# Optimization experiments

Measured on AMD Instinct MI355X. Metric: run time of the kernel, lower is better.

Reference implementation:

```python
import jax, jax.numpy as jnp
import numpy as np

B, L1, L2, DIN, H, DK, DV = 16, 1024, 1024, 1024, 16, 64, 64


def setup_inputs() -> dict:
    key = jax.random.key(0)
    ks = jax.random.split(key, 9)
    s = 1.0 / np.sqrt(DIN)
    return {
        "x": jax.random.normal(ks[0], (B, L1, DIN), dtype=jnp.float32),
        "y": jax.random.normal(ks[1], (B, L2, DIN), dtype=jnp.float32),
        "y_mask": jax.random.randint(ks[2], (B, L2), 0, 2) == 1,  # True => masked
        "Wq": jax.random.normal(ks[3], (DIN, H * DK), dtype=jnp.float32) * s,
        "bq": jnp.zeros((H * DK,), dtype=jnp.float32),
        "Wk": jax.random.normal(ks[4], (DIN, H * DK), dtype=jnp.float32) * s,
        "bk": jnp.zeros((H * DK,), dtype=jnp.float32),
        "Wv": jax.random.normal(ks[5], (DIN, H * DV), dtype=jnp.float32) * s,
        "bv": jnp.zeros((H * DV,), dtype=jnp.float32),
    }


def reference(x, y, y_mask, Wq, bq, Wk, bk, Wv, bv):
    b, l1, _ = x.shape
    l2 = y.shape[1]
    # QKV projections, split into heads: [b, len, H, d]
    q = (x @ Wq + bq).reshape(b, l1, H, DK)
    k = (y @ Wk + bk).reshape(b, l2, H, DK)
    v = (y @ Wv + bv).reshape(b, l2, H, DV)
    # (do_relu=False -> no relu)
    scores = jnp.einsum("bqhd,bkhd->bhqk", q, k) / jnp.sqrt(jnp.float32(DK))
    scores = jnp.where(y_mask[:, None, None, :], -jnp.inf, scores)
    alpha = jax.nn.softmax(scores, axis=-1)  # over len2
    out = jnp.einsum("bhqk,bkhd->bqhd", alpha, v)
    return out.reshape(b, l1, H * DV)
```

## Files before the change

kernel.cpp:

```cpp
#include <hip/hip_runtime.h>
#include <hip/hip_bf16.h>

#define BATCH 16
#define L1D 1024
#define L2D 1024
#define DIN 1024
#define NH 16
#define HD 1024

typedef __attribute__((ext_vector_type(4))) float floatx4;
typedef __attribute__((ext_vector_type(8))) short shortx8;
typedef __attribute__((ext_vector_type(8))) unsigned short ushortx8;
typedef __attribute__((ext_vector_type(4))) unsigned short ushortx4;

#if __has_builtin(__builtin_amdgcn_exp2f)
#define EXP2(x) __builtin_amdgcn_exp2f(x)
#else
#define EXP2(x) exp2f(x)
#endif

static __device__ __forceinline__ unsigned short f2bf(float f) {
    union { float f; unsigned u; } v; v.f = f;
    unsigned r = v.u + 0x7fff + ((v.u >> 16) & 1);
    return (unsigned short)(r >> 16);
}
static __device__ __forceinline__ unsigned short f2bf_fast(float f) {
    union { float f; unsigned u; } v; v.f = f;
    return (unsigned short)((v.u + 0x8000u) >> 16);
}

#define GLOBAL_AS __attribute__((address_space(1)))
#define LDS_AS __attribute__((address_space(3)))
static __device__ __forceinline__ void gl2lds16(const unsigned short* g, unsigned short* l) {
    __builtin_amdgcn_global_load_lds((const GLOBAL_AS unsigned int*)g,
                                     (LDS_AS unsigned int*)l, 16, 0, 0);
}

__global__ void cvt_kernel(const float* __restrict__ in, unsigned short* __restrict__ out) {
    size_t i = ((size_t)blockIdx.x * 256 + threadIdx.x) * 8;
    float4 a = *(const float4*)(in + i);
    float4 b = *(const float4*)(in + i + 4);
    ushortx8 o;
    o[0] = f2bf(a.x); o[1] = f2bf(a.y); o[2] = f2bf(a.z); o[3] = f2bf(a.w);
    o[4] = f2bf(b.x); o[5] = f2bf(b.y); o[6] = f2bf(b.z); o[7] = f2bf(b.w);
    *(ushortx8*)(out + i) = o;
}

__global__ void bias_kernel(const int* __restrict__ ym, float* __restrict__ bias) {
    int i = blockIdx.x * 256 + threadIdx.x;
    bias[i] = ym[i] ? -INFINITY : 0.0f;
}

__global__ void wt_kernel(const float* __restrict__ W, unsigned short* __restrict__ Wt) {
    __shared__ float tile[32][33];
    int bx = blockIdx.x, by = blockIdx.y;
    int tx = threadIdx.x, ty = threadIdx.y;
    for (int i = 0; i < 4; i++)
        tile[ty + i * 8][tx] = W[(size_t)(by * 32 + ty + i * 8) * HD + bx * 32 + tx];
    __syncthreads();
    for (int i = 0; i < 4; i++)
        Wt[(size_t)(bx * 32 + ty + i * 8) * DIN + by * 32 + tx] = f2bf(tile[tx][ty + i * 8]);
}

__global__ __launch_bounds__(256, 2) void gemm_kernel(
    const unsigned short* __restrict__ A, const unsigned short* __restrict__ Bt,
    const float* __restrict__ bias, unsigned short* __restrict__ Out, float scale)
{
    __shared__ unsigned short As[128 * 32];
    __shared__ unsigned short Bs[128 * 32];
    const int m0 = blockIdx.y * 128;
    const int n0 = blockIdx.x * 128;
    const int tid = threadIdx.x;
    const int wid = tid >> 6, lane = tid & 63;
    const int c = lane & 15, qd = lane >> 4;
    const int wm = (wid >> 1) * 64, wn = (wid & 1) * 64;

    floatx4 acc[4][4] = {};

    for (int k0 = 0; k0 < DIN; k0 += 32) {
        for (int i = 0; i < 2; i++) {
            int f16 = i * 256 + tid;
            int row = f16 >> 2;
            int cb  = (f16 & 3) * 8;
            gl2lds16(A  + (size_t)(m0 + row) * DIN + k0 + cb, &As[f16 * 8]);
            gl2lds16(Bt + (size_t)(n0 + row) * DIN + k0 + cb, &Bs[f16 * 8]);
        }
        __syncthreads();

        shortx8 a[4], b[4];
        for (int mt = 0; mt < 4; mt++)
            a[mt] = *(shortx8*)(&As[(wm + mt * 16 + c) * 32 + qd * 8]);
        for (int nt = 0; nt < 4; nt++)
            b[nt] = *(shortx8*)(&Bs[(wn + nt * 16 + c) * 32 + qd * 8]);
        for (int mt = 0; mt < 4; mt++)
            for (int nt = 0; nt < 4; nt++)
                acc[mt][nt] = __builtin_amdgcn_mfma_f32_16x16x32_bf16(
                    a[mt], b[nt], acc[mt][nt], 0, 0, 0);
        __syncthreads();
    }

    for (int nt = 0; nt < 4; nt++) {
        int gn = n0 + wn + nt * 16 + c;
        float bv = bias[gn];
        for (int mt = 0; mt < 4; mt++)
            for (int r = 0; r < 4; r++) {
                int gm = m0 + wm + mt * 16 + qd * 4 + r;
                Out[(size_t)gm * HD + gn] = f2bf((acc[mt][nt][r] + bv) * scale);
            }
    }
}

__global__ void vt_kernel(const unsigned short* __restrict__ V,
                          unsigned short* __restrict__ Vt) {
    __shared__ unsigned short t[64][72];
    const int l20 = blockIdx.x * 64;
    const int bh  = blockIdx.y;
    const int b = bh >> 4, h = bh & 15;
    const int tid = threadIdx.x;
    for (int i = 0; i < 2; i++) {
        int idx = i * 256 + tid;
        int row = idx >> 3, col = (idx & 7) * 8;
        *(ushortx8*)(&t[row][col]) =
            *(const ushortx8*)(V + (size_t)(b * L2D + l20 + row) * HD + h * 64 + col);
    }
    __syncthreads();
    for (int i = 0; i < 2; i++) {
        int idx = i * 256 + tid;
        int dv = idx >> 3, col = (idx & 7) * 8;
        ushortx8 v;
        for (int j = 0; j < 8; j++) v[j] = t[col + j][dv];
        *(ushortx8*)(Vt + (size_t)(bh * 64 + dv) * L2D + l20 + col) = v;
    }
}

__global__ __launch_bounds__(256, 4) void attn_kernel(
    const unsigned short* __restrict__ Q, const unsigned short* __restrict__ K,
    const unsigned short* __restrict__ Vt, const float* __restrict__ biasf,
    float* __restrict__ out)
{
    __shared__ unsigned short Ks[64 * 72];
    __shared__ unsigned short Vs[64 * 72];
    __shared__ unsigned short Ps[4][32 * 72];

    const int q0  = blockIdx.x * 128;
    const int bh  = blockIdx.y;
    const int b = bh >> 4, h = bh & 15;
    const int tid = threadIdx.x, wid = tid >> 6, lane = tid & 63;
    const int c = lane & 15, qd = lane >> 4;

    shortx8 qf[2][2];
    for (int mt2 = 0; mt2 < 2; mt2++)
        for (int kt = 0; kt < 2; kt++)
            qf[mt2][kt] = *(const shortx8*)(Q +
                (size_t)(b * L1D + q0 + wid * 32 + mt2 * 16 + c) * HD + h * 64 + kt * 32 + qd * 8);

    floatx4 o[2][4] = {};
    float psum[2][4] = {};

    const unsigned short* Kbase = K + (size_t)b * L2D * HD + h * 64;
    const unsigned short* Vbase = Vt + (size_t)bh * 64 * L2D;
    const float* bb = biasf + b * L2D;

    for (int kv0 = 0; kv0 < L2D; kv0 += 64) {
        for (int i = 0; i < 2; i++) {
            int idx = i * 256 + tid;
            int row = idx >> 3, col = (idx & 7) * 8;
            *(ushortx8*)(&Ks[row * 72 + col]) =
                *(const ushortx8*)(Kbase + (size_t)(kv0 + row) * HD + col);
            *(ushortx8*)(&Vs[row * 72 + col]) =
                *(const ushortx8*)(Vbase + (size_t)row * L2D + kv0 + col);
        }
        __syncthreads();

        float bv[4];
        for (int nt = 0; nt < 4; nt++) bv[nt] = bb[kv0 + nt * 16 + c];

        for (int mt2 = 0; mt2 < 2; mt2++) {
            for (int nt = 0; nt < 4; nt++) {
                floatx4 z = {};
                for (int kt = 0; kt < 2; kt++) {
                    shortx8 kf = *(shortx8*)(&Ks[(nt * 16 + c) * 72 + kt * 32 + qd * 8]);
                    z = __builtin_amdgcn_mfma_f32_16x16x32_bf16(qf[mt2][kt], kf, z, 0, 0, 0);
                }
                for (int r = 0; r < 4; r++) {
                    float p = EXP2(z[r] + bv[nt]);
                    psum[mt2][r] += p;
                    Ps[wid][(mt2 * 16 + qd * 4 + r) * 72 + nt * 16 + c] = f2bf_fast(p);
                }
            }
        }
        for (int mt2 = 0; mt2 < 2; mt2++) {
            shortx8 pf[2];
            for (int kt = 0; kt < 2; kt++)
                pf[kt] = *(shortx8*)(&Ps[wid][(mt2 * 16 + c) * 72 + kt * 32 + qd * 8]);
            for (int nt = 0; nt < 4; nt++)
                for (int kt = 0; kt < 2; kt++) {
                    shortx8 vf = *(shortx8*)(&Vs[(nt * 16 + c) * 72 + kt * 32 + qd * 8]);
                    o[mt2][nt] = __builtin_amdgcn_mfma_f32_16x16x32_bf16(pf[kt], vf, o[mt2][nt], 0, 0, 0);
                }
        }
        __syncthreads();
    }

    for (int mt2 = 0; mt2 < 2; mt2++)
        for (int r = 0; r < 4; r++) {
            float l = psum[mt2][r];
            for (int off = 1; off < 16; off <<= 1)
                l += __shfl_xor(l, off, 64);
            float inv = 1.0f / l;
            size_t rowbase = ((size_t)b * L1D + q0 + wid * 32 + mt2 * 16 + qd * 4 + r) * HD + h * 64;
            for (int nt = 0; nt < 4; nt++)
                out[rowbase + nt * 16 + c] = o[mt2][nt][r] * inv;
        }
}

extern "C" void kernel_launch(void* const* d_in, const int* in_sizes, int n_in,
                              void* d_out, int out_size, void* d_ws, size_t ws_size,
                              hipStream_t stream) {
    const float* x  = (const float*)d_in[0];
    const float* y  = (const float*)d_in[1];
    const int*  ym  = (const int*)d_in[2];
    const float* Wq = (const float*)d_in[3];
    const float* bq = (const float*)d_in[4];
    const float* Wk = (const float*)d_in[5];
    const float* bk = (const float*)d_in[6];
    const float* Wv = (const float*)d_in[7];
    const float* bv = (const float*)d_in[8];
    float* outp = (float*)d_out;

    const size_t M = (size_t)BATCH * L1D;
    const size_t T = M * HD;
    unsigned short* Qb  = (unsigned short*)d_ws;
    unsigned short* Kb  = Qb + T;
    unsigned short* Vb  = Kb + T;
    unsigned short* S1  = Vb + T;
    unsigned short* S2  = S1 + T;
    unsigned short* Wt  = S2 + T;
    float* biasf        = (float*)(Wt + (size_t)DIN * HD);

    const float QSCALE = 0.125f * 1.44269504088896340736f;

    cvt_kernel<<<T / 2048, 256, 0, stream>>>(x, S1);
    cvt_kernel<<<T / 2048, 256, 0, stream>>>(y, S2);
    bias_kernel<<<(BATCH * L2D) / 256, 256, 0, stream>>>(ym, biasf);

    dim3 wtg(HD / 32, DIN / 32), wtb(32, 8);
    dim3 gg(HD / 128, M / 128);
    wt_kernel<<<wtg, wtb, 0, stream>>>(Wq, Wt);
    gemm_kernel<<<gg, 256, 0, stream>>>(S1, Wt, bq, Qb, QSCALE);
    wt_kernel<<<wtg, wtb, 0, stream>>>(Wk, Wt);
    gemm_kernel<<<gg, 256, 0, stream>>>(S2, Wt, bk, Kb, 1.0f);
    wt_kernel<<<wtg, wtb, 0, stream>>>(Wv, Wt);
    gemm_kernel<<<gg, 256, 0, stream>>>(S2, Wt, bv, Vb, 1.0f);

    vt_kernel<<<dim3(L2D / 64, BATCH * NH), 256, 0, stream>>>(Vb, S1);

    attn_kernel<<<dim3(L1D / 128, BATCH * NH), 256, 0, stream>>>(Qb, Kb, S1, biasf, outp);
}
```

Before: 473.7 us.

## Fuse QKV GEMMs and prep kernels, swizzle LDS, async loads in attention

Merges the x/y conversion and mask-bias kernels into one launch, transposes all three weights in one launch, and computes Q, K and V with a single GEMM over a 3072-wide concatenated output. GEMM and attention LDS tiles use XOR swizzles instead of padding, and attention loads K/V tiles with direct global-to-LDS loads. Attention blocks are remapped so neighbouring blocks share heads for cache locality. This reduces launch overhead and bank conflicts, at the cost of a strided 3072-wide QKV layout.

```diff
diff --git a/kernel.cpp b/kernel.cpp
--- a/kernel.cpp
+++ b/kernel.cpp
@@ -7,11 +7,11 @@
 #define DIN 1024
 #define NH 16
 #define HD 1024
+#define OHD 3072
 
 typedef __attribute__((ext_vector_type(4))) float floatx4;
 typedef __attribute__((ext_vector_type(8))) short shortx8;
 typedef __attribute__((ext_vector_type(8))) unsigned short ushortx8;
-typedef __attribute__((ext_vector_type(4))) unsigned short ushortx4;
 
 #if __has_builtin(__builtin_amdgcn_exp2f)
 #define EXP2(x) __builtin_amdgcn_exp2f(x)
@@ -36,62 +36,81 @@
                                      (LDS_AS unsigned int*)l, 16, 0, 0);
 }
 
-__global__ void cvt_kernel(const float* __restrict__ in, unsigned short* __restrict__ out) {
-    size_t i = ((size_t)blockIdx.x * 256 + threadIdx.x) * 8;
-    float4 a = *(const float4*)(in + i);
-    float4 b = *(const float4*)(in + i + 4);
-    ushortx8 o;
-    o[0] = f2bf(a.x); o[1] = f2bf(a.y); o[2] = f2bf(a.z); o[3] = f2bf(a.w);
-    o[4] = f2bf(b.x); o[5] = f2bf(b.y); o[6] = f2bf(b.z); o[7] = f2bf(b.w);
-    *(ushortx8*)(out + i) = o;
-}
-
-__global__ void bias_kernel(const int* __restrict__ ym, float* __restrict__ bias) {
-    int i = blockIdx.x * 256 + threadIdx.x;
-    bias[i] = ym[i] ? -INFINITY : 0.0f;
-}
-
-__global__ void wt_kernel(const float* __restrict__ W, unsigned short* __restrict__ Wt) {
+#define NCVT 8192
+__global__ void prep_kernel(const float* __restrict__ x, const float* __restrict__ y,
+                            unsigned short* __restrict__ xb, unsigned short* __restrict__ yb,
+                            const int* __restrict__ ym, float* __restrict__ biasf) {
+    int bid = blockIdx.x;
+    if (bid < 2 * NCVT) {
+        const float* in = bid < NCVT ? x : y;
+        unsigned short* o = bid < NCVT ? xb : yb;
+        int bb = bid < NCVT ? bid : bid - NCVT;
+        size_t i = ((size_t)bb * 256 + threadIdx.x) * 8;
+        float4 a = *(const float4*)(in + i);
+        float4 b = *(const float4*)(in + i + 4);
+        ushortx8 v;
+        v[0] = f2bf(a.x); v[1] = f2bf(a.y); v[2] = f2bf(a.z); v[3] = f2bf(a.w);
+        v[4] = f2bf(b.x); v[5] = f2bf(b.y); v[6] = f2bf(b.z); v[7] = f2bf(b.w);
+        *(ushortx8*)(o + i) = v;
+    } else {
+        int i = (bid - 2 * NCVT) * 256 + threadIdx.x;
+        biasf[i] = ym[i] ? -INFINITY : 0.0f;
+    }
+}
+
+__global__ void wt_kernel(const float* __restrict__ Wq, const float* __restrict__ Wk,
+                          const float* __restrict__ Wv, unsigned short* __restrict__ Wt) {
     __shared__ float tile[32][33];
+    const float* W = blockIdx.z == 0 ? Wq : (blockIdx.z == 1 ? Wk : Wv);
+    unsigned short* dst = Wt + (size_t)blockIdx.z * HD * DIN;
     int bx = blockIdx.x, by = blockIdx.y;
     int tx = threadIdx.x, ty = threadIdx.y;
     for (int i = 0; i < 4; i++)
         tile[ty + i * 8][tx] = W[(size_t)(by * 32 + ty + i * 8) * HD + bx * 32 + tx];
     __syncthreads();
     for (int i = 0; i < 4; i++)
-        Wt[(size_t)(bx * 32 + ty + i * 8) * DIN + by * 32 + tx] = f2bf(tile[tx][ty + i * 8]);
+        dst[(size_t)(bx * 32 + ty + i * 8) * DIN + by * 32 + tx] = f2bf(tile[tx][ty + i * 8]);
 }
 
 __global__ __launch_bounds__(256, 2) void gemm_kernel(
-    const unsigned short* __restrict__ A, const unsigned short* __restrict__ Bt,
-    const float* __restrict__ bias, unsigned short* __restrict__ Out, float scale)
+    const unsigned short* __restrict__ xb, const unsigned short* __restrict__ yb,
+    const unsigned short* __restrict__ Wt,
+    const float* __restrict__ bq, const float* __restrict__ bk, const float* __restrict__ bvp,
+    unsigned short* __restrict__ Out, float qscale)
 {
     __shared__ unsigned short As[128 * 32];
     __shared__ unsigned short Bs[128 * 32];
+    const int n0 = blockIdx.x * 128;
     const int m0 = blockIdx.y * 128;
-    const int n0 = blockIdx.x * 128;
+    const int sec = n0 >> 10;
+    const unsigned short* A = (sec == 0) ? xb : yb;
+    const float* bias = (sec == 0) ? bq : (sec == 1 ? bk : bvp);
+    const float scale = (sec == 0) ? qscale : 1.0f;
+
     const int tid = threadIdx.x;
     const int wid = tid >> 6, lane = tid & 63;
     const int c = lane & 15, qd = lane >> 4;
     const int wm = (wid >> 1) * 64, wn = (wid & 1) * 64;
 
+    int f16a = tid, f16b = 256 + tid;
+    int rowA = f16a >> 2, scA = ((f16a & 3) ^ ((rowA >> 1) & 3)) * 8;
+    int rowB = f16b >> 2, scB = ((f16b & 3) ^ ((rowB >> 1) & 3)) * 8;
+    const int swz = (qd ^ ((c >> 1) & 3)) * 8;
+
     floatx4 acc[4][4] = {};
 
     for (int k0 = 0; k0 < DIN; k0 += 32) {
-        for (int i = 0; i < 2; i++) {
-            int f16 = i * 256 + tid;
-            int row = f16 >> 2;
-            int cb  = (f16 & 3) * 8;
-            gl2lds16(A  + (size_t)(m0 + row) * DIN + k0 + cb, &As[f16 * 8]);
-            gl2lds16(Bt + (size_t)(n0 + row) * DIN + k0 + cb, &Bs[f16 * 8]);
-        }
+        gl2lds16(A  + (size_t)(m0 + rowA) * DIN + k0 + scA, &As[f16a * 8]);
+        gl2lds16(Wt + (size_t)(n0 + rowA) * DIN + k0 + scA, &Bs[f16a * 8]);
+        gl2lds16(A  + (size_t)(m0 + rowB) * DIN + k0 + scB, &As[f16b * 8]);
+        gl2lds16(Wt + (size_t)(n0 + rowB) * DIN + k0 + scB, &Bs[f16b * 8]);
         __syncthreads();
 
         shortx8 a[4], b[4];
         for (int mt = 0; mt < 4; mt++)
-            a[mt] = *(shortx8*)(&As[(wm + mt * 16 + c) * 32 + qd * 8]);
+            a[mt] = *(shortx8*)(&As[(wm + mt * 16 + c) * 32 + swz]);
         for (int nt = 0; nt < 4; nt++)
-            b[nt] = *(shortx8*)(&Bs[(wn + nt * 16 + c) * 32 + qd * 8]);
+            b[nt] = *(shortx8*)(&Bs[(wn + nt * 16 + c) * 32 + swz]);
         for (int mt = 0; mt < 4; mt++)
             for (int nt = 0; nt < 4; nt++)
                 acc[mt][nt] = __builtin_amdgcn_mfma_f32_16x16x32_bf16(
@@ -101,11 +120,11 @@
 
     for (int nt = 0; nt < 4; nt++) {
         int gn = n0 + wn + nt * 16 + c;
-        float bv = bias[gn];
+        float bv = bias[gn & 1023];
         for (int mt = 0; mt < 4; mt++)
             for (int r = 0; r < 4; r++) {
                 int gm = m0 + wm + mt * 16 + qd * 4 + r;
-                Out[(size_t)gm * HD + gn] = f2bf((acc[mt][nt][r] + bv) * scale);
+                Out[(size_t)gm * OHD + gn] = f2bf((acc[mt][nt][r] + bv) * scale);
             }
     }
 }
@@ -121,7 +140,7 @@
         int idx = i * 256 + tid;
         int row = idx >> 3, col = (idx & 7) * 8;
         *(ushortx8*)(&t[row][col]) =
-            *(const ushortx8*)(V + (size_t)(b * L2D + l20 + row) * HD + h * 64 + col);
+            *(const ushortx8*)(V + (size_t)(b * L2D + l20 + row) * OHD + h * 64 + col);
     }
     __syncthreads();
     for (int i = 0; i < 2; i++) {
@@ -134,16 +153,17 @@
 }
 
 __global__ __launch_bounds__(256, 4) void attn_kernel(
-    const unsigned short* __restrict__ Q, const unsigned short* __restrict__ K,
+    const unsigned short* __restrict__ QK,
     const unsigned short* __restrict__ Vt, const float* __restrict__ biasf,
     float* __restrict__ out)
 {
-    __shared__ unsigned short Ks[64 * 72];
-    __shared__ unsigned short Vs[64 * 72];
+    __shared__ unsigned short Ks[64 * 64];
+    __shared__ unsigned short Vs[64 * 64];
     __shared__ unsigned short Ps[4][32 * 72];
 
-    const int q0  = blockIdx.x * 128;
-    const int bh  = blockIdx.y;
+    int f = blockIdx.y * gridDim.x + blockIdx.x;
+    int bh = (f & 7) * 32 + (f >> 6);
+    int q0 = ((f >> 3) & 7) * 128;
     const int b = bh >> 4, h = bh & 15;
     const int tid = threadIdx.x, wid = tid >> 6, lane = tid & 63;
     const int c = lane & 15, qd = lane >> 4;
@@ -151,25 +171,26 @@
     shortx8 qf[2][2];
     for (int mt2 = 0; mt2 < 2; mt2++)
         for (int kt = 0; kt < 2; kt++)
-            qf[mt2][kt] = *(const shortx8*)(Q +
-                (size_t)(b * L1D + q0 + wid * 32 + mt2 * 16 + c) * HD + h * 64 + kt * 32 + qd * 8);
+            qf[mt2][kt] = *(const shortx8*)(QK +
+                (size_t)(b * L1D + q0 + wid * 32 + mt2 * 16 + c) * OHD + h * 64 + kt * 32 + qd * 8);
 
     floatx4 o[2][4] = {};
     float psum[2][4] = {};
 
-    const unsigned short* Kbase = K + (size_t)b * L2D * HD + h * 64;
+    const unsigned short* Kbase = QK + HD + (size_t)b * L2D * OHD + h * 64;
     const unsigned short* Vbase = Vt + (size_t)bh * 64 * L2D;
     const float* bb = biasf + b * L2D;
 
+    int idxa = tid, idxb = 256 + tid;
+    int rowa = idxa >> 3, sca = ((idxa & 7) ^ (rowa & 7)) * 8;
+    int rowb = idxb >> 3, scb = ((idxb & 7) ^ (rowb & 7)) * 8;
+    const int swz8 = c & 7;
+
     for (int kv0 = 0; kv0 < L2D; kv0 += 64) {
-        for (int i = 0; i < 2; i++) {
-            int idx = i * 256 + tid;
-            int row = idx >> 3, col = (idx & 7) * 8;
-            *(ushortx8*)(&Ks[row * 72 + col]) =
-                *(const ushortx8*)(Kbase + (size_t)(kv0 + row) * HD + col);
-            *(ushortx8*)(&Vs[row * 72 + col]) =
-                *(const ushortx8*)(Vbase + (size_t)row * L2D + kv0 + col);
-        }
+        gl2lds16(Kbase + (size_t)(kv0 + rowa) * OHD + sca, &Ks[idxa * 8]);
+        gl2lds16(Vbase + (size_t)rowa * L2D + kv0 + sca, &Vs[idxa * 8]);
+        gl2lds16(Kbase + (size_t)(kv0 + rowb) * OHD + scb, &Ks[idxb * 8]);
+        gl2lds16(Vbase + (size_t)rowb * L2D + kv0 + scb, &Vs[idxb * 8]);
         __syncthreads();
 
         float bv[4];
@@ -179,7 +200,7 @@
             for (int nt = 0; nt < 4; nt++) {
                 floatx4 z = {};
                 for (int kt = 0; kt < 2; kt++) {
-                    shortx8 kf = *(shortx8*)(&Ks[(nt * 16 + c) * 72 + kt * 32 + qd * 8]);
+                    shortx8 kf = *(shortx8*)(&Ks[(nt * 16 + c) * 64 + ((kt * 4 + qd) ^ swz8) * 8]);
                     z = __builtin_amdgcn_mfma_f32_16x16x32_bf16(qf[mt2][kt], kf, z, 0, 0, 0);
                 }
                 for (int r = 0; r < 4; r++) {
@@ -195,7 +216,7 @@
                 pf[kt] = *(shortx8*)(&Ps[wid][(mt2 * 16 + c) * 72 + kt * 32 + qd * 8]);
             for (int nt = 0; nt < 4; nt++)
                 for (int kt = 0; kt < 2; kt++) {
-                    shortx8 vf = *(shortx8*)(&Vs[(nt * 16 + c) * 72 + kt * 32 + qd * 8]);
+                    shortx8 vf = *(shortx8*)(&Vs[(nt * 16 + c) * 64 + ((kt * 4 + qd) ^ swz8) * 8]);
                     o[mt2][nt] = __builtin_amdgcn_mfma_f32_16x16x32_bf16(pf[kt], vf, o[mt2][nt], 0, 0, 0);
                 }
         }
@@ -230,30 +251,17 @@
 
     const size_t M = (size_t)BATCH * L1D;
     const size_t T = M * HD;
-    unsigned short* Qb  = (unsigned short*)d_ws;
-    unsigned short* Kb  = Qb + T;
-    unsigned short* Vb  = Kb + T;
-    unsigned short* S1  = Vb + T;
-    unsigned short* S2  = S1 + T;
-    unsigned short* Wt  = S2 + T;
-    float* biasf        = (float*)(Wt + (size_t)DIN * HD);
+    unsigned short* Obuf = (unsigned short*)d_ws;
+    unsigned short* xb   = Obuf + M * OHD;
+    unsigned short* yb   = xb + T;
+    unsigned short* Wt   = yb + T;
+    float* biasf         = (float*)(Wt + (size_t)OHD * DIN);
 
     const float QSCALE = 0.125f * 1.44269504088896340736f;
 
-    cvt_kernel<<<T / 2048, 256, 0, stream>>>(x, S1);
-    cvt_kernel<<<T / 2048, 256, 0, stream>>>(y, S2);
-    bias_kernel<<<(BATCH * L2D) / 256, 256, 0, stream>>>(ym, biasf);
-
-    dim3 wtg(HD / 32, DIN / 32), wtb(32, 8);
-    dim3 gg(HD / 128, M / 128);
-    wt_kernel<<<wtg, wtb, 0, stream>>>(Wq, Wt);
-    gemm_kernel<<<gg, 256, 0, stream>>>(S1, Wt, bq, Qb, QSCALE);
-    wt_kernel<<<wtg, wtb, 0, stream>>>(Wk, Wt);
-    gemm_kernel<<<gg, 256, 0, stream>>>(S2, Wt, bk, Kb, 1.0f);
-    wt_kernel<<<wtg, wtb, 0, stream>>>(Wv, Wt);
-    gemm_kernel<<<gg, 256, 0, stream>>>(S2, Wt, bv, Vb, 1.0f);
-
-    vt_kernel<<<dim3(L2D / 64, BATCH * NH), 256, 0, stream>>>(Vb, S1);
-
-    attn_kernel<<<dim3(L1D / 128, BATCH * NH), 256, 0, stream>>>(Qb, Kb, S1, biasf, outp);
-}
+    prep_kernel<<<2 * NCVT + (BATCH * L2D) / 256, 256, 0, stream>>>(x, y, xb, yb, ym, biasf);
+    wt_kernel<<<dim3(HD / 32, DIN / 32, 3), dim3(32, 8), 0, stream>>>(Wq, Wk, Wv, Wt);
+    gemm_kernel<<<dim3(OHD / 128, M / 128), 256, 0, stream>>>(xb, yb, Wt, bq, bk, bv, Obuf, QSCALE);
+    vt_kernel<<<dim3(L2D / 64, BATCH * NH), 256, 0, stream>>>(Obuf + 2 * HD, xb);
+    attn_kernel<<<dim3(L1D / 128, BATCH * NH), 256, 0, stream>>>(Obuf, xb, biasf, outp);
+}
```

New measurement: 419.6 us. 11.4% less time.
